# Optimization experiments

Measured on AMD Instinct MI355X. Metric: run time of the kernel, lower is better.

The kernel has to match this reference:

```python
import jax, jax.numpy as jnp
import numpy as np

N_SRC = 16384
N_NBR = 16384
E = 524288
D = 128
ALPHA = 0.2  # leaky_relu slope


def setup_inputs() -> dict:
    key = jax.random.key(0)
    ks = jax.random.split(key, 16)
    s = lambda k, shape, fan: jax.random.normal(k, shape, jnp.float32) / np.sqrt(fan)
    x_cur = jax.random.normal(ks[0], (N_SRC, D), jnp.float32)
    x_nbr = jax.random.normal(ks[1], (N_NBR, D), jnp.float32)
    W1c = s(ks[2], (D, D), D); b1c = jnp.zeros((D,), jnp.float32)
    W2c = s(ks[3], (D, D), D); b2c = jnp.zeros((D,), jnp.float32)
    W1n = s(ks[4], (D, D), D); b1n = jnp.zeros((D,), jnp.float32)
    W2n = s(ks[5], (D, D), D); b2n = jnp.zeros((D,), jnp.float32)
    Wa = s(ks[6], (2 * D, 1), 2 * D); ba = jnp.zeros((1,), jnp.float32)
    src = jax.random.randint(ks[7], (E,), 0, N_SRC, jnp.int32)
    dst = jax.random.randint(ks[8], (E,), 0, N_NBR, jnp.int32)
    edges = jnp.stack([src, dst], axis=1)  # [E, 2]
    return dict(x_cur=x_cur, x_nbr=x_nbr, W1c=W1c, b1c=b1c, W2c=W2c, b2c=b2c,
                W1n=W1n, b1n=b1n, W2n=W2n, b2n=b2n, Wa=Wa, ba=ba, edges=edges)


def reference(x_cur, x_nbr, W1c, b1c, W2c, b2c, W1n, b1n, W2n, b2n, Wa, ba, edges):
    src, dst = edges[:, 0], edges[:, 1]
    # hidden MLPs (keras Dense with default activation=None -> linear stack)
    cur = (x_cur @ W1c + b1c) @ W2c + b2c          # [N_src, D]
    nbr = (x_nbr @ W1n + b1n) @ W2n + b2n          # [N_nbr, D]
    # per-edge gather + concat + attention MLP
    pair = jnp.concatenate([cur[src], nbr[dst]], axis=1)   # [E, 2D]
    scores = jax.nn.leaky_relu((pair @ Wa + ba)[:, 0], ALPHA)  # [E]
    # segment softmax over source node
    exp_s = jnp.exp(scores)
    seg_sum = jax.ops.segment_sum(exp_s, src, num_segments=N_SRC)  # [N_src]
    norm_s = exp_s / seg_sum[src]                                   # [E]
    # scatter to dense adjacency and matmul (faithful to tf.scatter_nd + matmul)
    adj = jnp.zeros((N_SRC, N_NBR), jnp.float32).at[src, dst].add(norm_s)
    return adj @ nbr                                # [N_src, D]
```

## Files before the change

kernel.cpp:

```cpp
#include <hip/hip_runtime.h>
#include <hip/hip_bf16.h>

#define NSRC 16384
#define NNBR 16384
#define NE   524288
#define DDIM 128
#define ALPHA_C 0.2f
#define CAP 128

typedef __hip_bfloat16 bf16;

__device__ __forceinline__ float b2f(bf16 v) { return __bfloat162float(v); }
__device__ __forceinline__ float us2f(unsigned short u) {
    return __uint_as_float(((unsigned)u) << 16);
}
__device__ __forceinline__ unsigned short f2us(float f) {
    bf16 h = __float2bfloat16(f);
    return *reinterpret_cast<unsigned short*>(&h);
}
__device__ __forceinline__ float LD(const void* p, int i, bool f32) {
    return f32 ? ((const float*)p)[i] : b2f(((const bf16*)p)[i]);
}
__device__ __forceinline__ bool detect_f32(const unsigned short* xprobe, int t, int* s_flag) {
    if (t < 64) {
        int ex = (xprobe[2 * t] >> 7) & 0xFF;
        unsigned long long m = __ballot(ex >= 0xC0);
        if (t == 0) *s_flag = (__popcll(m) >= 2) ? 1 : 0;
    }
    __syncthreads();
    return *s_flag != 0;
}

__global__ __launch_bounds__(1024) void k_prep(const unsigned short* __restrict__ xprobe,
                             const void* __restrict__ W1c, const void* __restrict__ b1c,
                             const void* __restrict__ W2c, const void* __restrict__ b2c,
                             const void* __restrict__ W1n, const void* __restrict__ b1n,
                             const void* __restrict__ W2n, const void* __restrict__ b2n,
                             const void* __restrict__ Wa, const void* __restrict__ ba,
                             int* __restrict__ flagp, float* __restrict__ u_c,
                             float* __restrict__ wan, float* __restrict__ bn,
                             float* __restrict__ c0, float* __restrict__ baf,
                             float* __restrict__ M, int* __restrict__ cursor) {
    __shared__ int s_flag;
    __shared__ float tc[DDIM], wa_s[DDIM];
    __shared__ float sred[2];
    __shared__ float w1r[8][DDIM];
    int t = threadIdx.x;

    if (blockIdx.x == 17) {
#pragma unroll
        for (int i = 0; i < NSRC / 1024; i++) cursor[i * 1024 + t] = 0;
        return;
    }
    const bool f32 = detect_f32(xprobe, t, &s_flag);

    if (blockIdx.x != 0) {
        int i0 = (blockIdx.x - 1) * 8;
        int r = t >> 7, j = t & 127;
        w1r[r][j] = LD(W1n, (i0 + r) * DDIM + j, f32);
        __syncthreads();
        float s = 0.f;
        if (f32) {
            const float* p = (const float*)W2n + j;
#pragma unroll 8
            for (int k = 0; k < DDIM; k++) s += w1r[r][k] * p[k * DDIM];
        } else {
            const bf16* p = (const bf16*)W2n + j;
#pragma unroll 8
            for (int k = 0; k < DDIM; k++) s += w1r[r][k] * b2f(p[k * DDIM]);
        }
        M[(i0 + r) * DDIM + j] = s;
        return;
    }

    if (t == 0) { flagp[0] = f32 ? 1 : 0; baf[0] = LD(ba, 0, f32); }
    if (t < DDIM) wa_s[t] = LD(Wa, t, f32);
    else if (t < 2 * DDIM) wan[t - DDIM] = LD(Wa, t, f32);
    __syncthreads();

    int row = t >> 3, sub = t & 7, k0 = sub * 16;
    float s = 0.f, bb = 0.f;
    if (f32) {
        const float* w2c = (const float*)W2c + row * DDIM + k0;
        const float* b1nf = (const float*)b1n;
        const float* w2n = (const float*)W2n;
#pragma unroll
        for (int k = 0; k < 16; k++) {
            s  += w2c[k] * wa_s[k0 + k];
            bb += b1nf[k0 + k] * w2n[(k0 + k) * DDIM + row];
        }
    } else {
        const bf16* w2c = (const bf16*)W2c + row * DDIM + k0;
        const bf16* b1nh = (const bf16*)b1n;
        const bf16* w2n = (const bf16*)W2n;
#pragma unroll
        for (int k = 0; k < 16; k++) {
            s  += b2f(w2c[k]) * wa_s[k0 + k];
            bb += b2f(b1nh[k0 + k]) * b2f(w2n[(k0 + k) * DDIM + row]);
        }
    }
    s  += __shfl_xor(s, 1, 64);  s  += __shfl_xor(s, 2, 64);  s  += __shfl_xor(s, 4, 64);
    bb += __shfl_xor(bb, 1, 64); bb += __shfl_xor(bb, 2, 64); bb += __shfl_xor(bb, 4, 64);
    if (sub == 0) { tc[row] = s; bn[row] = bb + LD(b2n, row, f32); }
    __syncthreads();

    float u = 0.f;
    if (f32) {
        const float* w1c = (const float*)W1c + row * DDIM + k0;
#pragma unroll
        for (int k = 0; k < 16; k++) u += w1c[k] * tc[k0 + k];
    } else {
        const bf16* w1c = (const bf16*)W1c + row * DDIM + k0;
#pragma unroll
        for (int k = 0; k < 16; k++) u += b2f(w1c[k]) * tc[k0 + k];
    }
    u += __shfl_xor(u, 1, 64); u += __shfl_xor(u, 2, 64); u += __shfl_xor(u, 4, 64);
    if (sub == 0) u_c[row] = u;

    if (t < 128) {
        float v = LD(b1c, t, f32) * tc[t] + LD(b2c, t, f32) * wa_s[t];
#pragma unroll
        for (int o = 32; o > 0; o >>= 1) v += __shfl_down(v, o, 64);
        if ((t & 63) == 0) sred[t >> 6] = v;
    }
    __syncthreads();
    if (t == 0) c0[0] = sred[0] + sred[1];
}

__global__ __launch_bounds__(128) void k_main(const void* __restrict__ Xn,
                                              const void* __restrict__ Xc,
                                              const float* __restrict__ M,
                                              const float* __restrict__ bn,
                                              const float* __restrict__ wan,
                                              const float* __restrict__ u_c,
                                              const float* __restrict__ c0,
                                              const int* __restrict__ flagp,
                                              unsigned short* __restrict__ Y,
                                              float* __restrict__ a_nbr,
                                              float* __restrict__ a_cur) {
    bool f32 = flagp[0] != 0;
    int t = threadIdx.x;
    if (blockIdx.x >= NNBR / 16) {
        int gw = (blockIdx.x - NNBR / 16) * 2 + (t >> 6);
        int lane = t & 63;
        float v0, v1;
        if (f32) {
            float2 v = reinterpret_cast<const float2*>((const float*)Xc + (size_t)gw * DDIM)[lane];
            v0 = v.x; v1 = v.y;
        } else {
            unsigned v = reinterpret_cast<const unsigned*>((const unsigned short*)Xc + (size_t)gw * DDIM)[lane];
            v0 = us2f((unsigned short)(v & 0xffffu));
            v1 = us2f((unsigned short)(v >> 16));
        }
        float acc = v0 * u_c[2 * lane] + v1 * u_c[2 * lane + 1];
#pragma unroll
        for (int o = 32; o > 0; o >>= 1) acc += __shfl_down(acc, o, 64);
        if (lane == 0) a_cur[gw] = acc + c0[0];
        return;
    }
    __shared__ float xs[16][DDIM];
    int rg = t >> 5, cg = t & 31;
    int row0 = blockIdx.x * 16;
    if (f32) {
        const float4* px = reinterpret_cast<const float4*>((const float*)Xn + (size_t)row0 * DDIM);
#pragma unroll
        for (int q = 0; q < 4; q++) {
            int idx = q * 128 + t;
            float4 v = px[idx];
            int rr = idx >> 5, c = (idx & 31) * 4;
            xs[rr][c] = v.x; xs[rr][c + 1] = v.y; xs[rr][c + 2] = v.z; xs[rr][c + 3] = v.w;
        }
    } else {
        const ushort4* px = reinterpret_cast<const ushort4*>((const bf16*)Xn + (size_t)row0 * DDIM);
#pragma unroll
        for (int q = 0; q < 4; q++) {
            int idx = q * 128 + t;
            ushort4 v = px[idx];
            int rr = idx >> 5, c = (idx & 31) * 4;
            xs[rr][c] = us2f(v.x); xs[rr][c + 1] = us2f(v.y);
            xs[rr][c + 2] = us2f(v.z); xs[rr][c + 3] = us2f(v.w);
        }
    }
    __syncthreads();
    float acc[4][4];
    float4 bb = reinterpret_cast<const float4*>(bn)[cg];
#pragma unroll
    for (int rr = 0; rr < 4; rr++) {
        acc[rr][0] = bb.x; acc[rr][1] = bb.y; acc[rr][2] = bb.z; acc[rr][3] = bb.w;
    }
    const float4* Mp = reinterpret_cast<const float4*>(M) + cg;
#pragma unroll 4
    for (int k = 0; k < DDIM; k++) {
        float4 m4 = Mp[k * 32];
        float x0 = xs[rg * 4 + 0][k], x1 = xs[rg * 4 + 1][k];
        float x2 = xs[rg * 4 + 2][k], x3 = xs[rg * 4 + 3][k];
        acc[0][0] += x0 * m4.x; acc[0][1] += x0 * m4.y; acc[0][2] += x0 * m4.z; acc[0][3] += x0 * m4.w;
        acc[1][0] += x1 * m4.x; acc[1][1] += x1 * m4.y; acc[1][2] += x1 * m4.z; acc[1][3] += x1 * m4.w;
        acc[2][0] += x2 * m4.x; acc[2][1] += x2 * m4.y; acc[2][2] += x2 * m4.z; acc[2][3] += x2 * m4.w;
        acc[3][0] += x3 * m4.x; acc[3][1] += x3 * m4.y; acc[3][2] += x3 * m4.z; acc[3][3] += x3 * m4.w;
    }
    float4 wn = reinterpret_cast<const float4*>(wan)[cg];
#pragma unroll
    for (int rr = 0; rr < 4; rr++) {
        int row = row0 + rg * 4 + rr;
        ushort4 y;
        y.x = f2us(acc[rr][0]); y.y = f2us(acc[rr][1]);
        y.z = f2us(acc[rr][2]); y.w = f2us(acc[rr][3]);
        reinterpret_cast<ushort4*>(Y + (size_t)row * DDIM)[cg] = y;
        float v = acc[rr][0] * wn.x + acc[rr][1] * wn.y + acc[rr][2] * wn.z + acc[rr][3] * wn.w;
        v += __shfl_xor(v, 1, 64); v += __shfl_xor(v, 2, 64); v += __shfl_xor(v, 4, 64);
        v += __shfl_xor(v, 8, 64); v += __shfl_xor(v, 16, 64);
        if (cg == 0) a_nbr[row] = v;
    }
}

__global__ __launch_bounds__(256) void k_edge(const int2* __restrict__ edges2,
                          const float* __restrict__ a_cur, const float* __restrict__ a_nbr,
                          const float* __restrict__ baf, int* __restrict__ cursor,
                          int2* __restrict__ dw) {
    int e = blockIdx.x * blockDim.x + threadIdx.x;
    if (e >= NE) return;
    int2 ed = edges2[e];
    float sc = a_cur[ed.x] + a_nbr[ed.y] + baf[0];
    sc = sc > 0.f ? sc : ALPHA_C * sc;
    sc = fminf(sc, 80.f);
    float w = __expf(sc);
    int p = atomicAdd(cursor + ed.x, 1);
    if (p < CAP) dw[ed.x * CAP + p] = make_int2(ed.y, __float_as_int(w));
}

__global__ __launch_bounds__(256) void k_aggregate(const int* __restrict__ cursor,
                                                   const int2* __restrict__ dw,
                                                   const unsigned short* __restrict__ nbr,
                                                   float* __restrict__ out) {
    int gw = blockIdx.x * 4 + (threadIdx.x >> 6);
    int lane = threadIdx.x & 63;
    int g = lane >> 3;
    int sub = lane & 7;
    int cnt = cursor[gw];
    cnt = cnt < CAP ? cnt : CAP;
    const int2* dwp = dw + (size_t)gw * CAP;
    float acc[16];
#pragma unroll
    for (int k = 0; k < 16; k++) acc[k] = 0.f;
    float den = 0.f;

    if (cnt > 0) {
        int j = g;
        bool act = j < cnt;
        int2 e = act ? dwp[j] : make_int2(0, 0);
        uint4 v0 = make_uint4(0, 0, 0, 0), v1 = v0;
        if (act) {
            const uint4* p = reinterpret_cast<const uint4*>(nbr + (size_t)e.x * DDIM + sub * 16);
            v0 = p[0]; v1 = p[1];
        }
        for (int base = 0; base < cnt; base += 8) {
            int jn = base + 8 + g;
            bool actn = jn < cnt;
            int2 en = make_int2(0, 0);
            uint4 n0 = make_uint4(0, 0, 0, 0), n1 = n0;
            if (actn) {
                en = dwp[jn];
                const uint4* p = reinterpret_cast<const uint4*>(nbr + (size_t)en.x * DDIM + sub * 16);
                n0 = p[0]; n1 = p[1];
            }
            float w = act ? __int_as_float(e.y) : 0.f;
            den += w;
            acc[0]  += w * us2f((unsigned short)(v0.x & 0xffffu));
            acc[1]  += w * us2f((unsigned short)(v0.x >> 16));
            acc[2]  += w * us2f((unsigned short)(v0.y & 0xffffu));
            acc[3]  += w * us2f((unsigned short)(v0.y >> 16));
            acc[4]  += w * us2f((unsigned short)(v0.z & 0xffffu));
            acc[5]  += w * us2f((unsigned short)(v0.z >> 16));
            acc[6]  += w * us2f((unsigned short)(v0.w & 0xffffu));
            acc[7]  += w * us2f((unsigned short)(v0.w >> 16));
            acc[8]  += w * us2f((unsigned short)(v1.x & 0xffffu));
            acc[9]  += w * us2f((unsigned short)(v1.x >> 16));
            acc[10] += w * us2f((unsigned short)(v1.y & 0xffffu));
            acc[11] += w * us2f((unsigned short)(v1.y >> 16));
            acc[12] += w * us2f((unsigned short)(v1.z & 0xffffu));
            acc[13] += w * us2f((unsigned short)(v1.z >> 16));
            acc[14] += w * us2f((unsigned short)(v1.w & 0xffffu));
            acc[15] += w * us2f((unsigned short)(v1.w >> 16));
            e = en; v0 = n0; v1 = n1; act = actn;
        }
    }
#pragma unroll
    for (int k = 0; k < 16; k++) {
        acc[k] += __shfl_xor(acc[k], 8, 64);
        acc[k] += __shfl_xor(acc[k], 16, 64);
        acc[k] += __shfl_xor(acc[k], 32, 64);
    }
    den += __shfl_xor(den, 8, 64);
    den += __shfl_xor(den, 16, 64);
    den += __shfl_xor(den, 32, 64);
    float inv = den > 0.f ? 1.f / den : 0.f;
    if (g == 0) {
        float4* po = reinterpret_cast<float4*>(out + (size_t)gw * DDIM + sub * 16);
        po[0] = make_float4(acc[0] * inv, acc[1] * inv, acc[2] * inv, acc[3] * inv);
        po[1] = make_float4(acc[4] * inv, acc[5] * inv, acc[6] * inv, acc[7] * inv);
        po[2] = make_float4(acc[8] * inv, acc[9] * inv, acc[10] * inv, acc[11] * inv);
        po[3] = make_float4(acc[12] * inv, acc[13] * inv, acc[14] * inv, acc[15] * inv);
    }
}

extern "C" void kernel_launch(void* const* d_in, const int* in_sizes, int n_in,
                              void* d_out, int out_size, void* d_ws, size_t ws_size,
                              hipStream_t stream) {
    const void* x_cur = d_in[0];
    const void* x_nbr = d_in[1];
    const void* W1c = d_in[2];
    const void* b1c = d_in[3];
    const void* W2c = d_in[4];
    const void* b2c = d_in[5];
    const void* W1n = d_in[6];
    const void* b1n = d_in[7];
    const void* W2n = d_in[8];
    const void* b2n = d_in[9];
    const void* Wa  = d_in[10];
    const void* ba  = d_in[11];
    const int2* edges2 = (const int2*)d_in[12];
    float* out = (float*)d_out;

    char* w = (char*)d_ws;
    size_t off = 0;
    auto alloc = [&](size_t b) { size_t o = off; off = (off + b + 255) & ~(size_t)255; return o; };
    float* M      = (float*)(w + alloc(DDIM * DDIM * 4));
    float* u_c    = (float*)(w + alloc(DDIM * 4));
    float* wan    = (float*)(w + alloc(DDIM * 4));
    float* bn     = (float*)(w + alloc(DDIM * 4));
    float* c0     = (float*)(w + alloc(4));
    float* baf    = (float*)(w + alloc(4));
    int*   flag   = (int*)(w + alloc(4));
    float* a_cur  = (float*)(w + alloc(NSRC * 4));
    float* a_nbr  = (float*)(w + alloc(NNBR * 4));
    int* cursor   = (int*)(w + alloc(NSRC * 4));
    int2* dw      = (int2*)(w + alloc((size_t)NSRC * CAP * 8));
    unsigned short* nbr = (unsigned short*)(w + alloc((size_t)NNBR * DDIM * 2));

    k_prep<<<18, 1024, 0, stream>>>((const unsigned short*)x_cur, W1c, b1c, W2c, b2c,
                                    W1n, b1n, W2n, b2n, Wa, ba, flag, u_c, wan, bn, c0, baf,
                                    M, cursor);
    k_main<<<NNBR / 16 + NSRC / 2, 128, 0, stream>>>(x_nbr, x_cur, M, bn, wan, u_c, c0,
                                                     flag, nbr, a_nbr, a_cur);
    k_edge<<<NE / 256, 256, 0, stream>>>(edges2, a_cur, a_nbr, baf, cursor, dw);
    k_aggregate<<<NSRC / 4, 256, 0, stream>>>(cursor, dw, nbr, out);
}
```

Measured before the change: 162.8 us.

## Fuse edge bucketing into main kernel and compute attention weights during aggregation

Removes the separate edge kernel. The edge bucketing (atomic cursor plus storing the neighbour index) now runs as extra blocks in k_main, in parallel with the GEMM and a_cur work, and the bucket holds int indices instead of int2 pairs. k_aggregate recomputes the leaky-relu/exp score from a_cur and a_nbr on the fly, which adds a dependent gather of a_nbr per edge. The GEMM tile also grows from 16 to 32 rows per block, and each a_cur block now handles 8 rows. This cuts one launch and halves the bucket traffic, but it adds a gather latency in the aggregate loop and more register pressure in the GEMM.

```diff
diff --git a/kernel.cpp b/kernel.cpp
--- a/kernel.cpp
+++ b/kernel.cpp
@@ -7,6 +7,10 @@
 #define DDIM 128
 #define ALPHA_C 0.2f
 #define CAP 128
+
+#define GEMM_BLKS (NNBR / 32)
+#define ACUR_BLKS (NSRC / 8)
+#define SCAT_BLKS (NE / 512)
 
 typedef __hip_bfloat16 bf16;
 
@@ -135,36 +139,61 @@
                                               const float* __restrict__ u_c,
                                               const float* __restrict__ c0,
                                               const int* __restrict__ flagp,
+                                              const int2* __restrict__ edges2,
+                                              int* __restrict__ cursor,
+                                              int* __restrict__ bucket,
                                               unsigned short* __restrict__ Y,
                                               float* __restrict__ a_nbr,
                                               float* __restrict__ a_cur) {
+    int t = threadIdx.x;
+    int b = blockIdx.x;
+
+    if (b >= GEMM_BLKS + ACUR_BLKS) {
+        int e0 = (b - GEMM_BLKS - ACUR_BLKS) * 512 + t * 4;
+        int4 p0 = reinterpret_cast<const int4*>(edges2)[t + (b - GEMM_BLKS - ACUR_BLKS) * 256];
+        int4 p1 = reinterpret_cast<const int4*>(edges2)[t + (b - GEMM_BLKS - ACUR_BLKS) * 256 + 128];
+        (void)e0;
+        int p;
+        p = atomicAdd(cursor + p0.x, 1); if (p < CAP) bucket[p0.x * CAP + p] = p0.y;
+        p = atomicAdd(cursor + p0.z, 1); if (p < CAP) bucket[p0.z * CAP + p] = p0.w;
+        p = atomicAdd(cursor + p1.x, 1); if (p < CAP) bucket[p1.x * CAP + p] = p1.y;
+        p = atomicAdd(cursor + p1.z, 1); if (p < CAP) bucket[p1.z * CAP + p] = p1.w;
+        return;
+    }
+
     bool f32 = flagp[0] != 0;
-    int t = threadIdx.x;
-    if (blockIdx.x >= NNBR / 16) {
-        int gw = (blockIdx.x - NNBR / 16) * 2 + (t >> 6);
+    if (b >= GEMM_BLKS) {
+        int base = (b - GEMM_BLKS) * 8 + (t >> 6) * 4;
         int lane = t & 63;
-        float v0, v1;
-        if (f32) {
-            float2 v = reinterpret_cast<const float2*>((const float*)Xc + (size_t)gw * DDIM)[lane];
-            v0 = v.x; v1 = v.y;
-        } else {
-            unsigned v = reinterpret_cast<const unsigned*>((const unsigned short*)Xc + (size_t)gw * DDIM)[lane];
-            v0 = us2f((unsigned short)(v & 0xffffu));
-            v1 = us2f((unsigned short)(v >> 16));
-        }
-        float acc = v0 * u_c[2 * lane] + v1 * u_c[2 * lane + 1];
-#pragma unroll
-        for (int o = 32; o > 0; o >>= 1) acc += __shfl_down(acc, o, 64);
-        if (lane == 0) a_cur[gw] = acc + c0[0];
+        float cc = c0[0];
+        float w0 = u_c[2 * lane], w1 = u_c[2 * lane + 1];
+#pragma unroll
+        for (int it = 0; it < 4; it++) {
+            int gw = base + it;
+            float v0, v1;
+            if (f32) {
+                float2 v = reinterpret_cast<const float2*>((const float*)Xc + (size_t)gw * DDIM)[lane];
+                v0 = v.x; v1 = v.y;
+            } else {
+                unsigned v = reinterpret_cast<const unsigned*>((const unsigned short*)Xc + (size_t)gw * DDIM)[lane];
+                v0 = us2f((unsigned short)(v & 0xffffu));
+                v1 = us2f((unsigned short)(v >> 16));
+            }
+            float acc = v0 * w0 + v1 * w1;
+#pragma unroll
+            for (int o = 32; o > 0; o >>= 1) acc += __shfl_down(acc, o, 64);
+            if (lane == 0) a_cur[gw] = acc + cc;
+        }
         return;
     }
-    __shared__ float xs[16][DDIM];
+
+    __shared__ float xs[32][DDIM];
     int rg = t >> 5, cg = t & 31;
-    int row0 = blockIdx.x * 16;
+    int row0 = b * 32;
     if (f32) {
         const float4* px = reinterpret_cast<const float4*>((const float*)Xn + (size_t)row0 * DDIM);
 #pragma unroll
-        for (int q = 0; q < 4; q++) {
+        for (int q = 0; q < 8; q++) {
             int idx = q * 128 + t;
             float4 v = px[idx];
             int rr = idx >> 5, c = (idx & 31) * 4;
@@ -173,7 +202,7 @@
     } else {
         const ushort4* px = reinterpret_cast<const ushort4*>((const bf16*)Xn + (size_t)row0 * DDIM);
 #pragma unroll
-        for (int q = 0; q < 4; q++) {
+        for (int q = 0; q < 8; q++) {
             int idx = q * 128 + t;
             ushort4 v = px[idx];
             int rr = idx >> 5, c = (idx & 31) * 4;
@@ -182,27 +211,27 @@
         }
     }
     __syncthreads();
-    float acc[4][4];
+    float acc[8][4];
     float4 bb = reinterpret_cast<const float4*>(bn)[cg];
 #pragma unroll
-    for (int rr = 0; rr < 4; rr++) {
+    for (int rr = 0; rr < 8; rr++) {
         acc[rr][0] = bb.x; acc[rr][1] = bb.y; acc[rr][2] = bb.z; acc[rr][3] = bb.w;
     }
     const float4* Mp = reinterpret_cast<const float4*>(M) + cg;
 #pragma unroll 4
     for (int k = 0; k < DDIM; k++) {
         float4 m4 = Mp[k * 32];
-        float x0 = xs[rg * 4 + 0][k], x1 = xs[rg * 4 + 1][k];
-        float x2 = xs[rg * 4 + 2][k], x3 = xs[rg * 4 + 3][k];
-        acc[0][0] += x0 * m4.x; acc[0][1] += x0 * m4.y; acc[0][2] += x0 * m4.z; acc[0][3] += x0 * m4.w;
-        acc[1][0] += x1 * m4.x; acc[1][1] += x1 * m4.y; acc[1][2] += x1 * m4.z; acc[1][3] += x1 * m4.w;
-        acc[2][0] += x2 * m4.x; acc[2][1] += x2 * m4.y; acc[2][2] += x2 * m4.z; acc[2][3] += x2 * m4.w;
-        acc[3][0] += x3 * m4.x; acc[3][1] += x3 * m4.y; acc[3][2] += x3 * m4.z; acc[3][3] += x3 * m4.w;
+#pragma unroll
+        for (int rr = 0; rr < 8; rr++) {
+            float x = xs[rg * 8 + rr][k];
+            acc[rr][0] += x * m4.x; acc[rr][1] += x * m4.y;
+            acc[rr][2] += x * m4.z; acc[rr][3] += x * m4.w;
+        }
     }
     float4 wn = reinterpret_cast<const float4*>(wan)[cg];
 #pragma unroll
-    for (int rr = 0; rr < 4; rr++) {
-        int row = row0 + rg * 4 + rr;
+    for (int rr = 0; rr < 8; rr++) {
+        int row = row0 + rg * 8 + rr;
         ushort4 y;
         y.x = f2us(acc[rr][0]); y.y = f2us(acc[rr][1]);
         y.z = f2us(acc[rr][2]); y.w = f2us(acc[rr][3]);
@@ -214,23 +243,11 @@
     }
 }
 
-__global__ __launch_bounds__(256) void k_edge(const int2* __restrict__ edges2,
-                          const float* __restrict__ a_cur, const float* __restrict__ a_nbr,
-                          const float* __restrict__ baf, int* __restrict__ cursor,
-                          int2* __restrict__ dw) {
-    int e = blockIdx.x * blockDim.x + threadIdx.x;
-    if (e >= NE) return;
-    int2 ed = edges2[e];
-    float sc = a_cur[ed.x] + a_nbr[ed.y] + baf[0];
-    sc = sc > 0.f ? sc : ALPHA_C * sc;
-    sc = fminf(sc, 80.f);
-    float w = __expf(sc);
-    int p = atomicAdd(cursor + ed.x, 1);
-    if (p < CAP) dw[ed.x * CAP + p] = make_int2(ed.y, __float_as_int(w));
-}
-
 __global__ __launch_bounds__(256) void k_aggregate(const int* __restrict__ cursor,
-                                                   const int2* __restrict__ dw,
+                                                   const int* __restrict__ bucket,
+                                                   const float* __restrict__ a_cur,
+                                                   const float* __restrict__ a_nbr,
+                                                   const float* __restrict__ baf,
                                                    const unsigned short* __restrict__ nbr,
                                                    float* __restrict__ out) {
     int gw = blockIdx.x * 4 + (threadIdx.x >> 6);
@@ -239,7 +256,8 @@
     int sub = lane & 7;
     int cnt = cursor[gw];
     cnt = cnt < CAP ? cnt : CAP;
-    const int2* dwp = dw + (size_t)gw * CAP;
+    const int* bp = bucket + (size_t)gw * CAP;
+    float acb = a_cur[gw] + baf[0];
     float acc[16];
 #pragma unroll
     for (int k = 0; k < 16; k++) acc[k] = 0.f;
@@ -248,23 +266,28 @@
     if (cnt > 0) {
         int j = g;
         bool act = j < cnt;
-        int2 e = act ? dwp[j] : make_int2(0, 0);
+        int d = act ? bp[j] : 0;
+        float an = act ? a_nbr[d] : 0.f;
         uint4 v0 = make_uint4(0, 0, 0, 0), v1 = v0;
         if (act) {
-            const uint4* p = reinterpret_cast<const uint4*>(nbr + (size_t)e.x * DDIM + sub * 16);
+            const uint4* p = reinterpret_cast<const uint4*>(nbr + (size_t)d * DDIM + sub * 16);
             v0 = p[0]; v1 = p[1];
         }
         for (int base = 0; base < cnt; base += 8) {
             int jn = base + 8 + g;
             bool actn = jn < cnt;
-            int2 en = make_int2(0, 0);
+            int dn = 0; float ann = 0.f;
             uint4 n0 = make_uint4(0, 0, 0, 0), n1 = n0;
             if (actn) {
-                en = dwp[jn];
-                const uint4* p = reinterpret_cast<const uint4*>(nbr + (size_t)en.x * DDIM + sub * 16);
+                dn = bp[jn];
+                ann = a_nbr[dn];
+                const uint4* p = reinterpret_cast<const uint4*>(nbr + (size_t)dn * DDIM + sub * 16);
                 n0 = p[0]; n1 = p[1];
             }
-            float w = act ? __int_as_float(e.y) : 0.f;
+            float sc = acb + an;
+            sc = sc > 0.f ? sc : ALPHA_C * sc;
+            sc = fminf(sc, 80.f);
+            float w = act ? __expf(sc) : 0.f;
             den += w;
             acc[0]  += w * us2f((unsigned short)(v0.x & 0xffffu));
             acc[1]  += w * us2f((unsigned short)(v0.x >> 16));
@@ -282,7 +305,7 @@
             acc[13] += w * us2f((unsigned short)(v1.z >> 16));
             acc[14] += w * us2f((unsigned short)(v1.w & 0xffffu));
             acc[15] += w * us2f((unsigned short)(v1.w >> 16));
-            e = en; v0 = n0; v1 = n1; act = actn;
+            an = ann; v0 = n0; v1 = n1; act = actn;
         }
     }
 #pragma unroll
@@ -335,14 +358,13 @@
     float* a_cur  = (float*)(w + alloc(NSRC * 4));
     float* a_nbr  = (float*)(w + alloc(NNBR * 4));
     int* cursor   = (int*)(w + alloc(NSRC * 4));
-    int2* dw      = (int2*)(w + alloc((size_t)NSRC * CAP * 8));
+    int* bucket   = (int*)(w + alloc((size_t)NSRC * CAP * 4));
     unsigned short* nbr = (unsigned short*)(w + alloc((size_t)NNBR * DDIM * 2));
 
     k_prep<<<18, 1024, 0, stream>>>((const unsigned short*)x_cur, W1c, b1c, W2c, b2c,
                                     W1n, b1n, W2n, b2n, Wa, ba, flag, u_c, wan, bn, c0, baf,
                                     M, cursor);
-    k_main<<<NNBR / 16 + NSRC / 2, 128, 0, stream>>>(x_nbr, x_cur, M, bn, wan, u_c, c0,
-                                                     flag, nbr, a_nbr, a_cur);
-    k_edge<<<NE / 256, 256, 0, stream>>>(edges2, a_cur, a_nbr, baf, cursor, dw);
-    k_aggregate<<<NSRC / 4, 256, 0, stream>>>(cursor, dw, nbr, out);
-}
+    k_main<<<GEMM_BLKS + ACUR_BLKS + SCAT_BLKS, 128, 0, stream>>>(
+        x_nbr, x_cur, M, bn, wan, u_c, c0, flag, edges2, cursor, bucket, nbr, a_nbr, a_cur);
+    k_aggregate<<<NSRC / 4, 256, 0, stream>>>(cursor, bucket, a_cur, a_nbr, baf, nbr, out);
+}
```

Measured after the change: 157.5 us. 1.03x faster.
